# Optimization experiments

Measured on AMD Instinct MI355X. Metric: run time of the kernel, lower is better.

## Reference

```python
import jax, jax.numpy as jnp
import numpy as np
import math

B, T, N, E = 16, 12, 2000, 8000
D, GAT_HEADS, NHEAD, FF, L, HORIZON = 64, 4, 4, 128, 2, 3
M = B * N  # batched node count


def setup_inputs() -> dict:
    key = jax.random.key(0)
    ks = jax.random.split(key, 16)

    def nrm(k, shape, s=0.1):
        return jax.random.normal(k, shape, jnp.float32) * s

    return dict(
        x_seq=jax.random.normal(ks[0], (B, T, N), jnp.float32),
        edge_index=jax.random.randint(ks[1], (2, E), 0, N),
        # GATConv 1: in_dim=1 -> 4 heads x 8 = 32
        W1=nrm(ks[2], (1, 32)),
        att_src1=nrm(ks[3], (GAT_HEADS, 8)),
        att_dst1=nrm(ks[4], (GAT_HEADS, 8)),
        b1=jnp.zeros((32,), jnp.float32),
        # GATConv 2: 32 -> 4 heads x 16 = 64
        W2=nrm(ks[5], (32, 64)),
        att_src2=nrm(ks[6], (GAT_HEADS, 16)),
        att_dst2=nrm(ks[7], (GAT_HEADS, 16)),
        b2=jnp.zeros((64,), jnp.float32),
        # TransformerEncoder (post-LN, relu), stacked over L layers
        Wqkv=nrm(ks[8], (L, 3 * D, D)), bqkv=jnp.zeros((L, 3 * D), jnp.float32),
        Wo=nrm(ks[9], (L, D, D)), bo=jnp.zeros((L, D), jnp.float32),
        Wf1=nrm(ks[10], (L, FF, D)), bf1=jnp.zeros((L, FF), jnp.float32),
        Wf2=nrm(ks[11], (L, D, FF)), bf2=jnp.zeros((L, D), jnp.float32),
        g1=jnp.ones((L, D), jnp.float32), be1=jnp.zeros((L, D), jnp.float32),
        g2=jnp.ones((L, D), jnp.float32), be2=jnp.zeros((L, D), jnp.float32),
        # prediction head
        Wh=nrm(ks[12], (HORIZON, D)), bh=jnp.zeros((HORIZON,), jnp.float32),
    )


def _layer_norm(x, g, b, eps=1e-5):
    mu = x.mean(-1, keepdims=True)
    var = ((x - mu) ** 2).mean(-1, keepdims=True)
    return (x - mu) * jax.lax.rsqrt(var + eps) * g + b


def _gat(x, src, dst, W, a_src, a_dst, bias, H, C, num_nodes):
    # PyG GATConv (concat=True, eval mode). x: [M, in] -> [M, H*C]
    h = (x @ W).reshape(-1, H, C)                                  # [M,H,C]
    e = jax.nn.leaky_relu((h * a_src).sum(-1)[src] + (h * a_dst).sum(-1)[dst], 0.2)  # [Etot,H]
    m = jax.ops.segment_max(e, dst, num_segments=num_nodes)
    w = jnp.exp(e - m[dst])
    s = jax.ops.segment_sum(w, dst, num_segments=num_nodes)
    alpha = w / (s[dst] + 1e-16)
    out = jax.ops.segment_sum(h[src] * alpha[:, :, None], dst, num_segments=num_nodes)
    return out.reshape(-1, H * C) + bias


def _forward(x_seq, edge_index, W1, att_src1, att_dst1, b1, W2, att_src2, att_dst2, b2,
             Wqkv, bqkv, Wo, bo, Wf1, bf1, Wf2, bf2, g1, be1, g2, be2, Wh, bh):
    # batch edge index with per-graph node offsets, then add self loops (PyG default)
    offs = (jnp.arange(B) * N)[:, None]
    loops = jnp.arange(M)
    src = jnp.concatenate([(edge_index[0][None] + offs).reshape(-1), loops])
    dst = jnp.concatenate([(edge_index[1][None] + offs).reshape(-1), loops])

    xt = x_seq.transpose(1, 0, 2).reshape(T, M, 1)  # per-timestep node features

    def gnn_step(x):
        h = jax.nn.relu(_gat(x, src, dst, W1, att_src1, att_dst1, b1, GAT_HEADS, 8, M))
        return jax.nn.relu(_gat(h, src, dst, W2, att_src2, att_dst2, b2, GAT_HEADS, 16, M))

    seq = jax.vmap(gnn_step)(xt)  # [T, M, D]

    # sinusoidal positional encoding over time axis
    pos = jnp.arange(T, dtype=jnp.float32)[:, None]
    div = jnp.exp(jnp.arange(0, D, 2, dtype=jnp.float32) * (-math.log(10000.0) / D))
    pe = jnp.zeros((T, D), jnp.float32)
    pe = pe.at[:, 0::2].set(jnp.sin(pos * div)).at[:, 1::2].set(jnp.cos(pos * div))
    seq = seq + pe[:, None, :]

    hd = D // NHEAD
    scale = 1.0 / math.sqrt(hd)
    for i in range(L):  # post-LN transformer encoder layers
        qkv = seq @ Wqkv[i].T + bqkv[i]
        q, k, v = jnp.split(qkv, 3, axis=-1)
        q = q.reshape(T, M, NHEAD, hd)
        k = k.reshape(T, M, NHEAD, hd)
        v = v.reshape(T, M, NHEAD, hd)
        sc = jnp.einsum('tmhd,smhd->mhts', q, k) * scale  # [M,H,T,T]
        attn = jax.nn.softmax(sc, axis=-1)
        o = jnp.einsum('mhts,smhd->tmhd', attn, v).reshape(T, M, D)
        seq = _layer_norm(seq + (o @ Wo[i].T + bo[i]), g1[i], be1[i])
        ff = jax.nn.relu(seq @ Wf1[i].T + bf1[i]) @ Wf2[i].T + bf2[i]
        seq = _layer_norm(seq + ff, g2[i], be2[i])

    final = seq[-1]  # [M, D]
    return (final @ Wh.T + bh).reshape(B, N, HORIZON).transpose(0, 2, 1)  # [B, horizon, N]


def reference(x_seq, edge_index, W1, att_src1, att_dst1, b1, W2, att_src2, att_dst2, b2,
              Wqkv, bqkv, Wo, bo, Wf1, bf1, Wf2, bf2, g1, be1, g2, be2, Wh, bh):
    return _forward(x_seq, edge_index, W1, att_src1, att_dst1, b1, W2, att_src2, att_dst2, b2,
                    Wqkv, bqkv, Wo, bo, Wf1, bf1, Wf2, bf2, g1, be1, g2, be2, Wh, bh)
```

## Files before the change

kernel.cpp:

```cpp
#include <hip/hip_runtime.h>
#include <hip/hip_bf16.h>

#define B_ 16
#define T_ 12
#define N_ 2000
#define E_ 8000
#define M_ 32000
#define ETOT (B_*E_ + M_)
#define D_ 64

typedef __hip_bfloat16 bf16;
typedef unsigned short u16;
typedef __attribute__((ext_vector_type(8))) _Float16 half8;
typedef __attribute__((ext_vector_type(2))) _Float16 h2v;
typedef __attribute__((ext_vector_type(4))) float f32x4;

__device__ __forceinline__ float bfu(u16 u){ return __uint_as_float(((unsigned int)u)<<16); }
__device__ __forceinline__ u16 f2bu(float f){
  unsigned int x = __float_as_uint(f);
  x += 0x7FFFu + ((x >> 16) & 1u);
  return (u16)(x >> 16);
}
__device__ __forceinline__ u16 f2h(float f){
  _Float16 h = (_Float16)f; u16 r; __builtin_memcpy(&r, &h, 2); return r;
}
__device__ __forceinline__ float h2f(u16 u){
  _Float16 h; __builtin_memcpy(&h, &u, 2); return (float)h;
}
__device__ __forceinline__ h2v u2h(unsigned u){ h2v r; __builtin_memcpy(&r,&u,4); return r; }

__device__ __forceinline__ float redsel16(const float v[16], int m){
  float c8[8];
  #pragma unroll
  for(int i=0;i<8;i++){
    float send = (m&8)? v[i]   : v[i+8];
    float keep = (m&8)? v[i+8] : v[i];
    c8[i] = keep + __shfl_xor(send, 8);
  }
  float c4[4];
  #pragma unroll
  for(int i=0;i<4;i++){
    float send = (m&4)? c8[i]   : c8[i+4];
    float keep = (m&4)? c8[i+4] : c8[i];
    c4[i] = keep + __shfl_xor(send, 4);
  }
  float c2[2];
  #pragma unroll
  for(int i=0;i<2;i++){
    float send = (m&2)? c4[i]   : c4[i+2];
    float keep = (m&2)? c4[i+2] : c4[i];
    c2[i] = keep + __shfl_xor(send, 2);
  }
  float send = (m&1)? c2[0] : c2[1];
  float keep = (m&1)? c2[1] : c2[0];
  return keep + __shfl_xor(send, 1);
}

__global__ void k_prep(const float* __restrict__ Wqkv, const float* __restrict__ Wo,
                       const float* __restrict__ Wf1, const float* __restrict__ Wf2,
                       const float* __restrict__ W2g,
                       u16* __restrict__ wqB, u16* __restrict__ woB,
                       u16* __restrict__ w1B, u16* __restrict__ w2B,
                       float* __restrict__ peT, u16* __restrict__ w2gB){
  int i = blockIdx.x*256 + threadIdx.x;
  if(i < 24576){
    int l=i/12288, r=i-l*12288;
    int nt=r>>10, r2=r&1023, c=r2>>9, r3=r2&511, lane=r3>>3, jj=r3&7;
    int m=lane&15, q=lane>>4;
    wqB[i] = f2h(Wqkv[l*12288 + (nt*16+m)*64 + c*32 + q*8 + jj]);
  } else if(i < 32768){
    int k2=i-24576;
    int l=k2>>12, r=k2&4095;
    int nt=r>>10, r2=r&1023, c=r2>>9, r3=r2&511, lane=r3>>3, jj=r3&7;
    int m=lane&15, q=lane>>4;
    woB[k2] = f2h(Wo[l*4096 + (nt*16+m)*64 + c*32 + q*8 + jj]);
  } else if(i < 49152){
    int k2=i-32768;
    int l=k2>>13, r=k2&8191;
    int nt=r>>10, r2=r&1023, c=r2>>9, r3=r2&511, lane=r3>>3, jj=r3&7;
    int m=lane&15, q=lane>>4;
    w1B[k2] = f2h(Wf1[l*8192 + (nt*16+m)*64 + c*32 + q*8 + jj]);
  } else if(i < 65536){
    int k2=i-49152;
    int l=k2>>13, r=k2&8191;
    int nt=r>>11, r2=r&2047, c=r2>>9, r3=r2&511, lane=r3>>3, jj=r3&7;
    int m=lane&15, q=lane>>4;
    w2B[k2] = f2h(Wf2[l*8192 + (nt*16+m)*128 + c*32 + q*8 + jj]);
  } else {
    int i2 = i - 65536;
    if(i2 < 768){
      int t=i2>>6, ch=i2&63;
      float ang = (float)t * __expf(-0.14391156463f * (float)(ch & ~1));
      peT[i2] = (ch&1) ? __cosf(ang) : __sinf(ang);
    } else if(i2 < 768+2048){
      int i3 = i2-768;
      int nt=i3>>9, r=i3&511, lane=r>>3, j=r&7;
      int m=lane&15, q=lane>>4;
      w2gB[i3] = f2h(W2g[(q*8+j)*64 + nt*16 + m]);
    }
  }
}

__global__ void k_hist(const int* __restrict__ ei, int* __restrict__ deg){
  int e = blockIdx.x*256 + threadIdx.x; if(e>=ETOT) return;
  int dst;
  if (e < B_*E_){ int b = e / E_; int k = e - b*E_; dst = ei[E_ + k] + b*N_; }
  else dst = e - B_*E_;
  atomicAdd(&deg[dst], 1);
}

__global__ void k_scan1(const int* __restrict__ deg, int* __restrict__ offs, int* __restrict__ bsums){
  __shared__ int s[256];
  int tid = threadIdx.x; int g = blockIdx.x*256 + tid;
  s[tid] = deg[g]; __syncthreads();
  for(int off=1; off<256; off<<=1){
    int a = (tid>=off) ? s[tid-off] : 0; __syncthreads();
    s[tid] += a; __syncthreads();
  }
  offs[g+1] = s[tid];
  if(tid==255) bsums[blockIdx.x] = s[255];
}

__global__ void k_scan23(int* __restrict__ offs, const int* __restrict__ bsums){
  __shared__ int s[128];
  int tid = threadIdx.x; int g = blockIdx.x*256 + tid;
  if(tid<128) s[tid] = (tid<125) ? bsums[tid] : 0;
  __syncthreads();
  for(int off=1; off<128; off<<=1){
    int a = 0;
    if(tid<128 && tid>=off) a = s[tid-off];
    __syncthreads();
    if(tid<128) s[tid] += a;
    __syncthreads();
  }
  int boff = (blockIdx.x==0) ? 0 : s[blockIdx.x-1];
  offs[g+1] += boff;
  if(g==0) offs[0]=0;
}

__global__ void k_scatter(const int* __restrict__ ei, const int* __restrict__ offs,
                          int* __restrict__ cursor, int* __restrict__ csr){
  int e = blockIdx.x*256 + threadIdx.x; if(e>=ETOT) return;
  int srcl, dst;
  if (e < B_*E_){ int b=e/E_; int k=e-b*E_; srcl=ei[k]; dst=ei[E_+k]+b*N_; }
  else { dst = e - B_*E_; int b=dst/N_; srcl = dst - b*N_; }
  int pos = atomicAdd(&cursor[dst], 1);
  csr[offs[dst]+pos] = srcl;
}

__global__ __launch_bounds__(256) void k_gat12(
  const float* __restrict__ x_seq, const float* __restrict__ W1,
  const float* __restrict__ as1, const float* __restrict__ ad1, const float* __restrict__ b1,
  const float* __restrict__ as2, const float* __restrict__ ad2,
  const int* __restrict__ offs, const int* __restrict__ csr,
  const u16* __restrict__ w2gB,
  u16* __restrict__ h2u, float* __restrict__ asc, float* __restrict__ adc)
{
  int tid = threadIdx.x, w = tid>>6, lane = tid&63;
  int m = lane&15, q = lane>>4;
  int t = blockIdx.y;
  int node = blockIdx.x*64 + w*16 + m;
  unsigned un=(unsigned)node, b=un/N_, n=un-b*N_;

  const half8* wb = (const half8*)w2gB;
  half8 w2f0 = wb[0*64+lane], w2f1 = wb[1*64+lane],
        w2f2 = wb[2*64+lane], w2f3 = wb[3*64+lane];

  float sS[4], sD[4];
  #pragma unroll
  for(int h=0;h<4;h++){
    float a=0.f, d=0.f;
    #pragma unroll
    for(int c=0;c<8;c++){ float wv=W1[h*8+c]; a+=wv*as1[h*8+c]; d+=wv*ad1[h*8+c]; }
    sS[h]=a; sD[h]=d;
  }

  const float* xsl = x_seq + (size_t)(b*T_+t)*N_;
  float xm = xsl[n];
  int e0=offs[node], e1=offs[node+1];
  float sum[4]={0.f,0.f,0.f,0.f}, ax[4]={0.f,0.f,0.f,0.f};
  for(int e=e0+q; e<e1; e+=4){
    float xv = xsl[csr[e]];
    #pragma unroll
    for(int h=0;h<4;h++){
      float ee = xv*sS[h] + xm*sD[h]; ee = ee>0.f ? ee : 0.2f*ee;
      float wv = __expf(ee); sum[h]+=wv; ax[h]+=wv*xv;
    }
  }
  #pragma unroll
  for(int h=0;h<4;h++){
    sum[h] += __shfl_xor(sum[h],16); sum[h] += __shfl_xor(sum[h],32);
    ax[h]  += __shfl_xor(ax[h],16);  ax[h]  += __shfl_xor(ax[h],32);
  }
  float A = ax[q]/(sum[q]+1e-16f);

  half8 af;
  #pragma unroll
  for(int j=0;j<8;j++){
    float v = A*W1[q*8+j] + b1[q*8+j]; v = v>0.f?v:0.f;
    af[j] = (_Float16)v;
  }
  f32x4 ac0={0.f,0.f,0.f,0.f}, ac1=ac0, ac2=ac0, ac3=ac0;
  ac0 = __builtin_amdgcn_mfma_f32_16x16x32_f16(af, w2f0, ac0,0,0,0);
  ac1 = __builtin_amdgcn_mfma_f32_16x16x32_f16(af, w2f1, ac1,0,0,0);
  ac2 = __builtin_amdgcn_mfma_f32_16x16x32_f16(af, w2f2, ac2,0,0,0);
  ac3 = __builtin_amdgcn_mfma_f32_16x16x32_f16(af, w2f3, ac3,0,0,0);

  size_t hbase = (size_t)t*M_;
  int ndbase = blockIdx.x*64 + w*16 + q*4;
  #pragma unroll
  for(int rg=0;rg<4;rg++){
    u16* row = h2u + (hbase + ndbase + rg)*64;
    row[ 0+m] = f2bu(ac0[rg]);
    row[16+m] = f2bu(ac1[rg]);
    row[32+m] = f2bu(ac2[rg]);
    row[48+m] = f2bu(ac3[rg]);
  }

  float a2sv[4], a2dv[4];
  #pragma unroll
  for(int h=0;h<4;h++){ a2sv[h]=as2[h*16+m]; a2dv[h]=ad2[h*16+m]; }
  float pa[16], pd[16];
  #pragma unroll
  for(int rg=0;rg<4;rg++){
    pa[0*4+rg]=ac0[rg]*a2sv[0]; pd[0*4+rg]=ac0[rg]*a2dv[0];
    pa[1*4+rg]=ac1[rg]*a2sv[1]; pd[1*4+rg]=ac1[rg]*a2dv[1];
    pa[2*4+rg]=ac2[rg]*a2sv[2]; pd[2*4+rg]=ac2[rg]*a2dv[2];
    pa[3*4+rg]=ac3[rg]*a2sv[3]; pd[3*4+rg]=ac3[rg]*a2dv[3];
  }
  float ra = redsel16(pa, m);
  float rd = redsel16(pd, m);
  {
    int h=m>>2, rg=m&3;
    size_t nd = hbase + ndbase + rg;
    asc[nd*4+h] = ra;
    adc[nd*4+h] = rd;
  }
}

__global__ __launch_bounds__(256) void k_gat2b(
  const u16* __restrict__ h2u, const float* __restrict__ asc, const float* __restrict__ adc,
  const float* __restrict__ b2, const int* __restrict__ offs, const int* __restrict__ csr,
  const float* __restrict__ peT, u16* __restrict__ seq)
{
  int t = blockIdx.y;
  int id = blockIdx.x*256 + threadIdx.x;
  int m = id>>2, h = id&3;
  unsigned um=(unsigned)m, b=um/N_;
  size_t base_s = (size_t)t*M_ + (size_t)b*N_;
  float am = adc[((size_t)t*M_+m)*4+h];
  int e0=offs[m], e1=offs[m+1];
  float sum=0.f;
  float A[16];
  #pragma unroll
  for(int c=0;c<16;c++) A[c]=0.f;
  for(int e=e0;e<e1;e++){
    size_t s = base_s + (unsigned)csr[e];
    float ee = asc[s*4+h] + am; ee = ee>0.f ? ee : 0.2f*ee;
    float w = __expf(ee); sum += w;
    const uint4* hp = (const uint4*)(h2u + s*64 + h*16);
    uint4 p0 = hp[0], p1 = hp[1];
    A[ 0] += w*bfu((u16)(p0.x)); A[ 1] += w*bfu((u16)(p0.x>>16));
    A[ 2] += w*bfu((u16)(p0.y)); A[ 3] += w*bfu((u16)(p0.y>>16));
    A[ 4] += w*bfu((u16)(p0.z)); A[ 5] += w*bfu((u16)(p0.z>>16));
    A[ 6] += w*bfu((u16)(p0.w)); A[ 7] += w*bfu((u16)(p0.w>>16));
    A[ 8] += w*bfu((u16)(p1.x)); A[ 9] += w*bfu((u16)(p1.x>>16));
    A[10] += w*bfu((u16)(p1.y)); A[11] += w*bfu((u16)(p1.y>>16));
    A[12] += w*bfu((u16)(p1.z)); A[13] += w*bfu((u16)(p1.z>>16));
    A[14] += w*bfu((u16)(p1.w)); A[15] += w*bfu((u16)(p1.w>>16));
  }
  float inv = 1.f/(sum + 1e-16f);
  u16 ov[16];
  #pragma unroll
  for(int c=0;c<16;c++){
    int ch = h*16 + c;
    float v = A[c]*inv + b2[ch]; v = v>0.f ? v : 0.f;
    ov[c] = f2h(v + peT[t*64+ch]);
  }
  uint4 o0, o1;
  o0.x = (unsigned)ov[0] | ((unsigned)ov[1]<<16);
  o0.y = (unsigned)ov[2] | ((unsigned)ov[3]<<16);
  o0.z = (unsigned)ov[4] | ((unsigned)ov[5]<<16);
  o0.w = (unsigned)ov[6] | ((unsigned)ov[7]<<16);
  o1.x = (unsigned)ov[8] | ((unsigned)ov[9]<<16);
  o1.y = (unsigned)ov[10]| ((unsigned)ov[11]<<16);
  o1.z = (unsigned)ov[12]| ((unsigned)ov[13]<<16);
  o1.w = (unsigned)ov[14]| ((unsigned)ov[15]<<16);
  uint4* op = (uint4*)(seq + ((size_t)t*M_ + m)*64 + h*16);
  op[0] = o0; op[1] = o1;
}

__global__ __launch_bounds__(192) void k_layer2(
  const u16* __restrict__ seq,
  const u16* __restrict__ wqB, const u16* __restrict__ woB,
  const u16* __restrict__ w1B, const u16* __restrict__ w2B,
  const float* __restrict__ bqkv, const float* __restrict__ bo,
  const float* __restrict__ bf1,  const float* __restrict__ bf2,
  const float* __restrict__ g1,   const float* __restrict__ be1,
  const float* __restrict__ g2,   const float* __restrict__ be2,
  const float* __restrict__ Wh,   const float* __restrict__ bh,
  float* __restrict__ out)
{
  __shared__ __align__(16) u16 X[3456];
  __shared__ __align__(16) u16 QKV[10368];
  u16* Hd = QKV + 3456;
  int tid=threadIdx.x, w=tid>>6, lane=tid&63;
  int m=lane&15, q=lane>>4;
  int r = w*16 + m;

  #pragma unroll
  for(int half=0; half<2; half++){
    int rr = half*8 + (lane>>3);
    int row = w*16 + rr;
    int nn = row/12, tt = row-nn*12;
    const uint4* src = (const uint4*)(seq + ((size_t)tt*M_ + (size_t)blockIdx.x*4+nn)*64) + (lane&7);
    *((uint4*)&X[row*72] + (lane&7)) = *src;
  }

  #pragma unroll 1
  for(int l=0; l<2; l++){
    const half8* wqv = (const half8*)(wqB + (size_t)l*12288);
    const half8* wov = (const half8*)(woB + (size_t)l*4096);
    const half8* w1v = (const half8*)(w1B + (size_t)l*8192);
    const half8* w2v = (const half8*)(w2B + (size_t)l*8192);
    const float* bq = bqkv + l*192;
    const float* boL = bo + l*64;
    const float* b1L = bf1 + l*128;
    const float* b2L = bf2 + l*64;
    const float* g1L = g1 + l*64, *be1L = be1 + l*64;
    const float* g2L = g2 + l*64, *be2L = be2 + l*64;

    half8 xa0 = *(const half8*)&X[r*72 + q*8];
    half8 xa1 = *(const half8*)&X[r*72 + 32 + q*8];
    #pragma unroll
    for(int nt=0; nt<12; nt++){
      f32x4 acc={0.f,0.f,0.f,0.f};
      acc = __builtin_amdgcn_mfma_f32_16x16x32_f16(xa0, wqv[(nt*2+0)*64+lane], acc,0,0,0);
      acc = __builtin_amdgcn_mfma_f32_16x16x32_f16(xa1, wqv[(nt*2+1)*64+lane], acc,0,0,0);
      int cg = nt*16+m; float bias = bq[cg];
      int s = nt>>2, lc = cg&63;
      #pragma unroll
      for(int rg=0;rg<4;rg++){
        int row = w*16 + q*4 + rg;
        QKV[s*3456 + row*72 + lc] = f2h(acc[rg]+bias);
      }
    }
    __syncthreads();

    {
      int an = tid/48, rem = tid - an*48;
      int ah = rem/12, at = rem - ah*12;
      u16* qrow = &QKV[(an*12+at)*72 + ah*16];
      uint4 qa = ((const uint4*)qrow)[0], qb = ((const uint4*)qrow)[1];
      float s[12];
      #pragma unroll
      for(int t2=0;t2<12;t2++){
        const uint4* kp = (const uint4*)&QKV[3456 + (an*12+t2)*72 + ah*16];
        uint4 ka=kp[0], kb=kp[1];
        float d=0.f;
        d=__builtin_amdgcn_fdot2(u2h(qa.x),u2h(ka.x),d,false);
        d=__builtin_amdgcn_fdot2(u2h(qa.y),u2h(ka.y),d,false);
        d=__builtin_amdgcn_fdot2(u2h(qa.z),u2h(ka.z),d,false);
        d=__builtin_amdgcn_fdot2(u2h(qa.w),u2h(ka.w),d,false);
        d=__builtin_amdgcn_fdot2(u2h(qb.x),u2h(kb.x),d,false);
        d=__builtin_amdgcn_fdot2(u2h(qb.y),u2h(kb.y),d,false);
        d=__builtin_amdgcn_fdot2(u2h(qb.z),u2h(kb.z),d,false);
        d=__builtin_amdgcn_fdot2(u2h(qb.w),u2h(kb.w),d,false);
        s[t2] = d*0.25f;
      }
      float mx=s[0];
      #pragma unroll
      for(int t2=1;t2<12;t2++) mx=fmaxf(mx,s[t2]);
      float sum=0.f;
      #pragma unroll
      for(int t2=0;t2<12;t2++){ s[t2]=__expf(s[t2]-mx); sum+=s[t2]; }
      float inv=1.f/sum;
      half8 o0, o1;
      #pragma unroll
      for(int i=0;i<8;i++){ o0[i]=(_Float16)0.f; o1[i]=(_Float16)0.f; }
      #pragma unroll
      for(int t2=0;t2<12;t2++){
        const half8* vr = (const half8*)&QKV[6912 + (an*12+t2)*72 + ah*16];
        _Float16 wh = (_Float16)s[t2];
        o0 += vr[0]*wh; o1 += vr[1]*wh;
      }
      _Float16 ih = (_Float16)inv;
      ((half8*)qrow)[0]=o0*ih; ((half8*)qrow)[1]=o1*ih;
    }
    __syncthreads();

    half8 oa0 = *(const half8*)&QKV[r*72 + q*8];
    half8 oa1 = *(const half8*)&QKV[r*72 + 32 + q*8];
    float y[4][4];
    #pragma unroll
    for(int nt=0;nt<4;nt++){
      f32x4 acc={0.f,0.f,0.f,0.f};
      acc = __builtin_amdgcn_mfma_f32_16x16x32_f16(oa0, wov[(nt*2+0)*64+lane], acc,0,0,0);
      acc = __builtin_amdgcn_mfma_f32_16x16x32_f16(oa1, wov[(nt*2+1)*64+lane], acc,0,0,0);
      int col=nt*16+m; float bias=boL[col];
      #pragma unroll
      for(int rg=0;rg<4;rg++)
        y[nt][rg] = acc[rg] + bias + h2f(X[(w*16+q*4+rg)*72 + col]);
    }
    float mu[4], rs[4];
    #pragma unroll
    for(int rg=0;rg<4;rg++){
      float sm=(y[0][rg]+y[1][rg])+(y[2][rg]+y[3][rg]);
      sm+=__shfl_xor(sm,1); sm+=__shfl_xor(sm,2); sm+=__shfl_xor(sm,4); sm+=__shfl_xor(sm,8);
      mu[rg]=sm*(1.f/64.f);
      float d0=y[0][rg]-mu[rg],d1=y[1][rg]-mu[rg],d2=y[2][rg]-mu[rg],d3=y[3][rg]-mu[rg];
      float vv=(d0*d0+d1*d1)+(d2*d2+d3*d3);
      vv+=__shfl_xor(vv,1); vv+=__shfl_xor(vv,2); vv+=__shfl_xor(vv,4); vv+=__shfl_xor(vv,8);
      rs[rg]=rsqrtf(vv*(1.f/64.f)+1e-5f);
    }
    #pragma unroll
    for(int nt=0;nt<4;nt++){
      int col=nt*16+m; float g=g1L[col], be=be1L[col];
      #pragma unroll
      for(int rg=0;rg<4;rg++){
        float v=(y[nt][rg]-mu[rg])*rs[rg]*g+be;
        y[nt][rg]=v;
        QKV[(w*16+q*4+rg)*72 + col]=f2h(v);
      }
    }

    half8 ya0 = *(const half8*)&QKV[r*72 + q*8];
    half8 ya1 = *(const half8*)&QKV[r*72 + 32 + q*8];
    #pragma unroll
    for(int nt=0;nt<8;nt++){
      f32x4 acc={0.f,0.f,0.f,0.f};
      acc = __builtin_amdgcn_mfma_f32_16x16x32_f16(ya0, w1v[(nt*2+0)*64+lane], acc,0,0,0);
      acc = __builtin_amdgcn_mfma_f32_16x16x32_f16(ya1, w1v[(nt*2+1)*64+lane], acc,0,0,0);
      float bias=b1L[nt*16+m];
      #pragma unroll
      for(int rg=0;rg<4;rg++)
        Hd[(w*16+q*4+rg)*136 + nt*16+m] = f2h(fmaxf(acc[rg]+bias, 0.f));
    }

    half8 ha[4];
    #pragma unroll
    for(int c=0;c<4;c++)
      ha[c] = *(const half8*)&Hd[r*136 + c*32 + q*8];
    #pragma unroll
    for(int nt=0;nt<4;nt++){
      f32x4 acc={0.f,0.f,0.f,0.f};
      #pragma unroll
      for(int c=0;c<4;c++)
        acc = __builtin_amdgcn_mfma_f32_16x16x32_f16(ha[c], w2v[(nt*4+c)*64+lane], acc,0,0,0);
      int col=nt*16+m; float bias=b2L[col];
      #pragma unroll
      for(int rg=0;rg<4;rg++)
        y[nt][rg] = acc[rg] + bias + y[nt][rg];
    }
    #pragma unroll
    for(int rg=0;rg<4;rg++){
      float sm=(y[0][rg]+y[1][rg])+(y[2][rg]+y[3][rg]);
      sm+=__shfl_xor(sm,1); sm+=__shfl_xor(sm,2); sm+=__shfl_xor(sm,4); sm+=__shfl_xor(sm,8);
      mu[rg]=sm*(1.f/64.f);
      float d0=y[0][rg]-mu[rg],d1=y[1][rg]-mu[rg],d2=y[2][rg]-mu[rg],d3=y[3][rg]-mu[rg];
      float vv=(d0*d0+d1*d1)+(d2*d2+d3*d3);
      vv+=__shfl_xor(vv,1); vv+=__shfl_xor(vv,2); vv+=__shfl_xor(vv,4); vv+=__shfl_xor(vv,8);
      rs[rg]=rsqrtf(vv*(1.f/64.f)+1e-5f);
    }
    if(l==0){
      #pragma unroll
      for(int nt=0;nt<4;nt++){
        int col=nt*16+m; float g=g2L[col], be=be2L[col];
        #pragma unroll
        for(int rg=0;rg<4;rg++)
          X[(w*16+q*4+rg)*72 + col] = f2h((y[nt][rg]-mu[rg])*rs[rg]*g + be);
      }
      __syncthreads();
    } else {
      int rc = w*16 + q*4 + 3;
      int nn = rc/12;
      if(rc - nn*12 == 11){
        float vfin[4];
        #pragma unroll
        for(int nt=0;nt<4;nt++){
          int col=nt*16+m;
          vfin[nt] = (y[nt][3]-mu[3])*rs[3]*g2L[col] + be2L[col];
        }
        int gm = blockIdx.x*4 + nn;
        unsigned bb=(unsigned)gm/N_, n2=(unsigned)gm-bb*N_;
        #pragma unroll
        for(int h3=0;h3<3;h3++){
          float p = vfin[0]*Wh[h3*64+m]    + vfin[1]*Wh[h3*64+16+m]
                  + vfin[2]*Wh[h3*64+32+m] + vfin[3]*Wh[h3*64+48+m];
          p += __shfl_xor(p,1); p += __shfl_xor(p,2);
          p += __shfl_xor(p,4); p += __shfl_xor(p,8);
          if(m==0) out[(bb*3+h3)*N_+n2] = p + bh[h3];
        }
      }
    }
  }
}

extern "C" void kernel_launch(void* const* d_in, const int* in_sizes, int n_in,
                              void* d_out, int out_size, void* d_ws, size_t ws_size,
                              hipStream_t stream)
{
  const float* x_seq=(const float*)d_in[0];
  const int*   ei   =(const int*)d_in[1];
  const float* W1   =(const float*)d_in[2];
  const float* as1  =(const float*)d_in[3];
  const float* ad1  =(const float*)d_in[4];
  const float* b1   =(const float*)d_in[5];
  const float* W2   =(const float*)d_in[6];
  const float* as2  =(const float*)d_in[7];
  const float* ad2  =(const float*)d_in[8];
  const float* b2   =(const float*)d_in[9];
  const float* Wqkv =(const float*)d_in[10];
  const float* bqkv =(const float*)d_in[11];
  const float* Wo   =(const float*)d_in[12];
  const float* bo   =(const float*)d_in[13];
  const float* Wf1  =(const float*)d_in[14];
  const float* bf1p =(const float*)d_in[15];
  const float* Wf2  =(const float*)d_in[16];
  const float* bf2p =(const float*)d_in[17];
  const float* g1   =(const float*)d_in[18];
  const float* be1  =(const float*)d_in[19];
  const float* g2   =(const float*)d_in[20];
  const float* be2  =(const float*)d_in[21];
  const float* Wh   =(const float*)d_in[22];
  const float* bh   =(const float*)d_in[23];

  u16* seqh   = (u16*)d_ws;
  float* asc  = (float*)(seqh + 24576000);
  float* adc  = asc + 1536000;
  int* deg    = (int*)(adc + 1536000);
  int* cursor = deg + M_;
  int* offs   = cursor + M_;
  int* bsums  = offs + (M_ + 2);
  int* boffs  = bsums + 128;
  int* csr    = boffs + 128;
  u16* h2u    = (u16*)(csr + ETOT);
  u16* wqB    = h2u + (size_t)T_*M_*64;
  u16* woB    = wqB + 24576;
  u16* w1B    = woB + 8192;
  u16* w2B    = w1B + 16384;
  float* peT  = (float*)(w2B + 16384);
  u16* w2gB   = (u16*)(peT + 768);

  k_prep   <<<dim3(268), dim3(256), 0, stream>>>(Wqkv, Wo, Wf1, Wf2, W2,
                                                 wqB, woB, w1B, w2B, peT, w2gB);

  hipMemsetAsync(deg, 0, (size_t)2*M_*sizeof(int), stream);
  k_hist   <<<dim3((ETOT+255)/256), dim3(256), 0, stream>>>(ei, deg);
  k_scan1  <<<dim3(125), dim3(256), 0, stream>>>(deg, offs, bsums);
  k_scan23 <<<dim3(125), dim3(256), 0, stream>>>(offs, bsums);
  k_scatter<<<dim3((ETOT+255)/256), dim3(256), 0, stream>>>(ei, offs, cursor, csr);

  k_gat12<<<dim3(500,T_), dim3(256), 0, stream>>>(x_seq, W1, as1, ad1, b1,
                                                  as2, ad2, offs, csr, w2gB,
                                                  h2u, asc, adc);
  k_gat2b<<<dim3(500,T_), dim3(256), 0, stream>>>(h2u, asc, adc, b2, offs, csr, peT, seqh);

  k_layer2<<<dim3(8000), dim3(192), 0, stream>>>(seqh,
      wqB, woB, w1B, w2B,
      bqkv, bo, bf1p, bf2p,
      g1, be1, g2, be2,
      Wh, bh, (float*)d_out);
}
```

Measured before the change: 374.5 us.

## Transpose GAT2 MFMA output layout and split edge loop across thread pairs

In k_gat12 the MFMA operands are swapped so each lane holds four consecutive channels of one node. That allows packed 8-byte row stores and replaces the 16-way select-shuffle reduction with a simple dot product plus two xor shuffles. In k_gat2b each (node, head) is now handled by two threads that stride over alternate edges, reduce partial sums with a shuffle, and each write half of the 16 output channels. The grid doubles to expose more parallelism and shorten per-thread serial gather loops, at the cost of extra shuffles and duplicated address/attention math. The code relies on a `node` variable defined in the hidden part of k_gat12 matching the transposed layout.

New measurement: 371.4 us. Within noise of the previous version (-0.8%).

```diff
diff --git a/kernel.cpp b/kernel.cpp
--- a/kernel.cpp
+++ b/kernel.cpp
@@ -28,33 +28,6 @@
   _Float16 h; __builtin_memcpy(&h, &u, 2); return (float)h;
 }
 __device__ __forceinline__ h2v u2h(unsigned u){ h2v r; __builtin_memcpy(&r,&u,4); return r; }
-
-__device__ __forceinline__ float redsel16(const float v[16], int m){
-  float c8[8];
-  #pragma unroll
-  for(int i=0;i<8;i++){
-    float send = (m&8)? v[i]   : v[i+8];
-    float keep = (m&8)? v[i+8] : v[i];
-    c8[i] = keep + __shfl_xor(send, 8);
-  }
-  float c4[4];
-  #pragma unroll
-  for(int i=0;i<4;i++){
-    float send = (m&4)? c8[i]   : c8[i+4];
-    float keep = (m&4)? c8[i+4] : c8[i];
-    c4[i] = keep + __shfl_xor(send, 4);
-  }
-  float c2[2];
-  #pragma unroll
-  for(int i=0;i<2;i++){
-    float send = (m&2)? c4[i]   : c4[i+2];
-    float keep = (m&2)? c4[i+2] : c4[i];
-    c2[i] = keep + __shfl_xor(send, 2);
-  }
-  float send = (m&1)? c2[0] : c2[1];
-  float keep = (m&1)? c2[1] : c2[0];
-  return keep + __shfl_xor(send, 1);
-}
 
 __global__ void k_prep(const float* __restrict__ Wqkv, const float* __restrict__ Wo,
                        const float* __restrict__ Wf1, const float* __restrict__ Wf2,
@@ -201,41 +174,49 @@
     af[j] = (_Float16)v;
   }
   f32x4 ac0={0.f,0.f,0.f,0.f}, ac1=ac0, ac2=ac0, ac3=ac0;
-  ac0 = __builtin_amdgcn_mfma_f32_16x16x32_f16(af, w2f0, ac0,0,0,0);
-  ac1 = __builtin_amdgcn_mfma_f32_16x16x32_f16(af, w2f1, ac1,0,0,0);
-  ac2 = __builtin_amdgcn_mfma_f32_16x16x32_f16(af, w2f2, ac2,0,0,0);
-  ac3 = __builtin_amdgcn_mfma_f32_16x16x32_f16(af, w2f3, ac3,0,0,0);
-
-  size_t hbase = (size_t)t*M_;
-  int ndbase = blockIdx.x*64 + w*16 + q*4;
-  #pragma unroll
-  for(int rg=0;rg<4;rg++){
-    u16* row = h2u + (hbase + ndbase + rg)*64;
-    row[ 0+m] = f2bu(ac0[rg]);
-    row[16+m] = f2bu(ac1[rg]);
-    row[32+m] = f2bu(ac2[rg]);
-    row[48+m] = f2bu(ac3[rg]);
-  }
-
-  float a2sv[4], a2dv[4];
-  #pragma unroll
-  for(int h=0;h<4;h++){ a2sv[h]=as2[h*16+m]; a2dv[h]=ad2[h*16+m]; }
-  float pa[16], pd[16];
-  #pragma unroll
-  for(int rg=0;rg<4;rg++){
-    pa[0*4+rg]=ac0[rg]*a2sv[0]; pd[0*4+rg]=ac0[rg]*a2dv[0];
-    pa[1*4+rg]=ac1[rg]*a2sv[1]; pd[1*4+rg]=ac1[rg]*a2dv[1];
-    pa[2*4+rg]=ac2[rg]*a2sv[2]; pd[2*4+rg]=ac2[rg]*a2dv[2];
-    pa[3*4+rg]=ac3[rg]*a2sv[3]; pd[3*4+rg]=ac3[rg]*a2dv[3];
-  }
-  float ra = redsel16(pa, m);
-  float rd = redsel16(pd, m);
+  ac0 = __builtin_amdgcn_mfma_f32_16x16x32_f16(w2f0, af, ac0,0,0,0);
+  ac1 = __builtin_amdgcn_mfma_f32_16x16x32_f16(w2f1, af, ac1,0,0,0);
+  ac2 = __builtin_amdgcn_mfma_f32_16x16x32_f16(w2f2, af, ac2,0,0,0);
+  ac3 = __builtin_amdgcn_mfma_f32_16x16x32_f16(w2f3, af, ac3,0,0,0);
+
+  size_t nd = (size_t)t*M_ + node;
+  u16* row = h2u + nd*64;
   {
-    int h=m>>2, rg=m&3;
-    size_t nd = hbase + ndbase + rg;
-    asc[nd*4+h] = ra;
-    adc[nd*4+h] = rd;
-  }
+    uint2 p;
+    p.x = (unsigned)f2bu(ac0[0]) | ((unsigned)f2bu(ac0[1])<<16);
+    p.y = (unsigned)f2bu(ac0[2]) | ((unsigned)f2bu(ac0[3])<<16);
+    *(uint2*)(row + 0*16 + q*4) = p;
+    p.x = (unsigned)f2bu(ac1[0]) | ((unsigned)f2bu(ac1[1])<<16);
+    p.y = (unsigned)f2bu(ac1[2]) | ((unsigned)f2bu(ac1[3])<<16);
+    *(uint2*)(row + 1*16 + q*4) = p;
+    p.x = (unsigned)f2bu(ac2[0]) | ((unsigned)f2bu(ac2[1])<<16);
+    p.y = (unsigned)f2bu(ac2[2]) | ((unsigned)f2bu(ac2[3])<<16);
+    *(uint2*)(row + 2*16 + q*4) = p;
+    p.x = (unsigned)f2bu(ac3[0]) | ((unsigned)f2bu(ac3[1])<<16);
+    p.y = (unsigned)f2bu(ac3[2]) | ((unsigned)f2bu(ac3[3])<<16);
+    *(uint2*)(row + 3*16 + q*4) = p;
+  }
+
+  const float* a2sp = as2 + q*4;
+  const float* a2dp = ad2 + q*4;
+  float ps[4], pd[4];
+  ps[0]=ac0[0]*a2sp[ 0]+ac0[1]*a2sp[ 1]+ac0[2]*a2sp[ 2]+ac0[3]*a2sp[ 3];
+  ps[1]=ac1[0]*a2sp[16]+ac1[1]*a2sp[17]+ac1[2]*a2sp[18]+ac1[3]*a2sp[19];
+  ps[2]=ac2[0]*a2sp[32]+ac2[1]*a2sp[33]+ac2[2]*a2sp[34]+ac2[3]*a2sp[35];
+  ps[3]=ac3[0]*a2sp[48]+ac3[1]*a2sp[49]+ac3[2]*a2sp[50]+ac3[3]*a2sp[51];
+  pd[0]=ac0[0]*a2dp[ 0]+ac0[1]*a2dp[ 1]+ac0[2]*a2dp[ 2]+ac0[3]*a2dp[ 3];
+  pd[1]=ac1[0]*a2dp[16]+ac1[1]*a2dp[17]+ac1[2]*a2dp[18]+ac1[3]*a2dp[19];
+  pd[2]=ac2[0]*a2dp[32]+ac2[1]*a2dp[33]+ac2[2]*a2dp[34]+ac2[3]*a2dp[35];
+  pd[3]=ac3[0]*a2dp[48]+ac3[1]*a2dp[49]+ac3[2]*a2dp[50]+ac3[3]*a2dp[51];
+  #pragma unroll
+  for(int h=0;h<4;h++){
+    ps[h] += __shfl_xor(ps[h],16); ps[h] += __shfl_xor(ps[h],32);
+    pd[h] += __shfl_xor(pd[h],16); pd[h] += __shfl_xor(pd[h],32);
+  }
+  float ra = (q&1) ? ((q&2)? ps[3]:ps[1]) : ((q&2)? ps[2]:ps[0]);
+  float rd = (q&1) ? ((q&2)? pd[3]:pd[1]) : ((q&2)? pd[2]:pd[0]);
+  asc[nd*4+q] = ra;
+  adc[nd*4+q] = rd;
 }
 
 __global__ __launch_bounds__(256) void k_gat2b(
@@ -245,7 +226,7 @@
 {
   int t = blockIdx.y;
   int id = blockIdx.x*256 + threadIdx.x;
-  int m = id>>2, h = id&3;
+  int m = id>>3, j = (id>>2)&1, h = id&3;
   unsigned um=(unsigned)m, b=um/N_;
   size_t base_s = (size_t)t*M_ + (size_t)b*N_;
   float am = adc[((size_t)t*M_+m)*4+h];
@@ -254,7 +235,7 @@
   float A[16];
   #pragma unroll
   for(int c=0;c<16;c++) A[c]=0.f;
-  for(int e=e0;e<e1;e++){
+  for(int e=e0+j; e<e1; e+=2){
     size_t s = base_s + (unsigned)csr[e];
     float ee = asc[s*4+h] + am; ee = ee>0.f ? ee : 0.2f*ee;
     float w = __expf(ee); sum += w;
@@ -269,25 +250,24 @@
     A[12] += w*bfu((u16)(p1.z)); A[13] += w*bfu((u16)(p1.z>>16));
     A[14] += w*bfu((u16)(p1.w)); A[15] += w*bfu((u16)(p1.w>>16));
   }
+  sum += __shfl_xor(sum,4);
+  #pragma unroll
+  for(int c=0;c<16;c++) A[c] += __shfl_xor(A[c],4);
+
   float inv = 1.f/(sum + 1e-16f);
-  u16 ov[16];
-  #pragma unroll
-  for(int c=0;c<16;c++){
-    int ch = h*16 + c;
-    float v = A[c]*inv + b2[ch]; v = v>0.f ? v : 0.f;
+  u16 ov[8];
+  #pragma unroll
+  for(int c=0;c<8;c++){
+    int ch = h*16 + j*8 + c;
+    float v = A[j*8+c]*inv + b2[ch]; v = v>0.f ? v : 0.f;
     ov[c] = f2h(v + peT[t*64+ch]);
   }
-  uint4 o0, o1;
-  o0.x = (unsigned)ov[0] | ((unsigned)ov[1]<<16);
-  o0.y = (unsigned)ov[2] | ((unsigned)ov[3]<<16);
-  o0.z = (unsigned)ov[4] | ((unsigned)ov[5]<<16);
-  o0.w = (unsigned)ov[6] | ((unsigned)ov[7]<<16);
-  o1.x = (unsigned)ov[8] | ((unsigned)ov[9]<<16);
-  o1.y = (unsigned)ov[10]| ((unsigned)ov[11]<<16);
-  o1.z = (unsigned)ov[12]| ((unsigned)ov[13]<<16);
-  o1.w = (unsigned)ov[14]| ((unsigned)ov[15]<<16);
-  uint4* op = (uint4*)(seq + ((size_t)t*M_ + m)*64 + h*16);
-  op[0] = o0; op[1] = o1;
+  uint4 o;
+  o.x = (unsigned)ov[0] | ((unsigned)ov[1]<<16);
+  o.y = (unsigned)ov[2] | ((unsigned)ov[3]<<16);
+  o.z = (unsigned)ov[4] | ((unsigned)ov[5]<<16);
+  o.w = (unsigned)ov[6] | ((unsigned)ov[7]<<16);
+  *(uint4*)(seq + ((size_t)t*M_ + m)*64 + h*16 + j*8) = o;
 }
 
 __global__ __launch_bounds__(192) void k_layer2(
@@ -554,7 +534,7 @@
   k_gat12<<<dim3(500,T_), dim3(256), 0, stream>>>(x_seq, W1, as1, ad1, b1,
                                                   as2, ad2, offs, csr, w2gB,
                                                   h2u, asc, adc);
-  k_gat2b<<<dim3(500,T_), dim3(256), 0, stream>>>(h2u, asc, adc, b2, offs, csr, peT, seqh);
+  k_gat2b<<<dim3(1000,T_), dim3(256), 0, stream>>>(h2u, asc, adc, b2, offs, csr, peT, seqh);
 
   k_layer2<<<dim3(8000), dim3(192), 0, stream>>>(seqh,
       wqB, woB, w1B, w2B,
```
